# Kernel optimization log

Hardware: AMD Instinct MI355X
Metric: run time of the kernel (lower is better)

Reference implementation:

```python
import jax, jax.numpy as jnp
import numpy as np

KH, KW = 3, 3
STRIDE, PAD, DIL = 1, 1, 1
HEADS, GROUPS, CLIP = 12, 12, 2
C, H, W = 288, 64, 64
B = 2


def _bilinear(img, ys, xs):
    # img: (c, H, W); ys, xs: (K, H, W) fractional sample coords -> (c, K, H, W)
    # DCN-style bilinear with zero outside the image (per-corner validity).
    Hh, Ww = img.shape[1], img.shape[2]
    y0 = jnp.floor(ys)
    x0 = jnp.floor(xs)
    dy = ys - y0
    dx = xs - x0
    out = jnp.zeros((img.shape[0],) + ys.shape, dtype=img.dtype)
    for oy, wy in ((y0, 1.0 - dy), (y0 + 1.0, dy)):
        for ox, wx in ((x0, 1.0 - dx), (x0 + 1.0, dx)):
            valid = (oy >= 0) & (oy <= Hh - 1) & (ox >= 0) & (ox <= Ww - 1)
            yi = jnp.clip(oy, 0, Hh - 1).astype(jnp.int32)
            xi = jnp.clip(ox, 0, Ww - 1).astype(jnp.int32)
            out = out + img[:, yi, xi] * (wy * wx * valid.astype(img.dtype))[None]
    return out


_sample = jax.vmap(jax.vmap(jax.vmap(_bilinear)))  # over (B, T, G)


def _linear5d(x, Wm, b):
    # x: (n, d, c, h, w); Wm: (out, in); torch nn.Linear applied channel-last
    return jnp.einsum('ndchw,oc->ndohw', x, Wm) + b[None, None, :, None, None]


def _deform_attn(q, kv, offset):
    # q: (B,1,C,H,W); kv: (B,T,2C,H,W); offset: (B, T*G*K*2, H, W)
    K = KH * KW
    hd = C // HEADS
    cpg = C // GROUPS
    scale = hd ** -0.5
    A = H * W
    off = offset.reshape(B, CLIP, GROUPS, K, 2, H, W)
    ky = jnp.repeat(jnp.arange(KH), KW).astype(q.dtype)   # (K,)
    kx = jnp.tile(jnp.arange(KW), KH).astype(q.dtype)
    py = jnp.arange(H, dtype=q.dtype)
    px = jnp.arange(W, dtype=q.dtype)
    base_y = ky[:, None, None] * DIL - PAD + py[None, :, None] * STRIDE  # (K,H,1)
    base_x = kx[:, None, None] * DIL - PAD + px[None, None, :] * STRIDE  # (K,1,W)
    ys = base_y + off[..., 0, :, :]  # (B,T,G,K,H,W)
    xs = base_x + off[..., 1, :, :]
    # split kv into k/v, group channels so k and v share per-group offsets
    k_in = kv[:, :, :C].reshape(B, CLIP, GROUPS, cpg, H, W)
    v_in = kv[:, :, C:].reshape(B, CLIP, GROUPS, cpg, H, W)
    kv_g = jnp.concatenate([k_in, v_in], axis=3)          # (B,T,G,2*cpg,H,W)
    samp = _sample(kv_g, ys, xs)                          # (B,T,G,2*cpg,K,H,W)
    k_s = samp[:, :, :, :cpg]
    v_s = samp[:, :, :, cpg:]
    # (B,T,G,cpg,K,H,W) -> (B,HEADS,hd,T*K,A)
    def to_heads(t):
        t = t.reshape(B, CLIP, C, K, A).transpose(0, 2, 1, 3, 4)
        return t.reshape(B, HEADS, hd, CLIP * K, A)
    k_s = to_heads(k_s)
    v_s = to_heads(v_s)
    q_r = q.reshape(B, HEADS, hd, A) * jnp.asarray(scale, q.dtype)
    attn = jnp.einsum('bhda,bhdka->bhka', q_r, k_s)       # (B,HEADS,T*K,A)
    attn = jax.nn.softmax(attn, axis=2)
    out = jnp.einsum('bhka,bhdka->bhda', attn, v_s)
    return out.reshape(B, 1, C, H, W)


def setup_inputs() -> dict:
    key = jax.random.key(0)
    ks = jax.random.split(key, 16)
    s = 0.02
    inp = {
        'q': jax.random.normal(ks[0], (B, 1, C, H, W), jnp.float32),
        'k': jax.random.normal(ks[1], (B, CLIP, C, H, W), jnp.float32),
        'v': jax.random.normal(ks[2], (B, CLIP, C, H, W), jnp.float32),
        'offset': jax.random.normal(ks[3], (B, CLIP * GROUPS * KH * KW * 2, H, W), jnp.float32),
        'Wq': jax.random.normal(ks[4], (C, C), jnp.float32) * s,
        'bq': jnp.zeros((C,), jnp.float32),
        'Wk': jax.random.normal(ks[5], (C, C), jnp.float32) * s,
        'bk': jnp.zeros((C,), jnp.float32),
        'Wv': jax.random.normal(ks[6], (C, C), jnp.float32) * s,
        'bv': jnp.zeros((C,), jnp.float32),
        'W1': jax.random.normal(ks[7], (2 * C, C), jnp.float32) * s,
        'b1': jnp.zeros((2 * C,), jnp.float32),
        'W2': jax.random.normal(ks[8], (C, 2 * C), jnp.float32) * s,
        'b2': jnp.zeros((C,), jnp.float32),
    }
    return inp


def reference(q, k, v, offset, Wq, bq, Wk, bk, Wv, bv, W1, b1, W2, b2):
    qp = _linear5d(q, Wq, bq)
    kv = jnp.concatenate([_linear5d(k, Wk, bk), _linear5d(v, Wv, bv)], axis=2)
    o = _deform_attn(qp, kv, offset)
    # MLP (channel-last), residual: v = v + mlp(v)
    x = jnp.moveaxis(o, 2, -1)
    x = jnp.einsum('ndhwc,oc->ndhwo', x, W1) + b1
    x = jax.nn.gelu(x, approximate=False)
    x = jnp.einsum('ndhwc,oc->ndhwo', x, W2) + b2
    return o + jnp.moveaxis(x, -1, 2)
```

## Files before the change

kernel.cpp:

```cpp
#include <hip/hip_runtime.h>

#define AREA 4096

typedef short short8 __attribute__((ext_vector_type(8)));
typedef float f32x4 __attribute__((ext_vector_type(4)));

__device__ __forceinline__ unsigned bf16_rn(float x) {
    unsigned u = __builtin_bit_cast(unsigned, x);
    u += 0x7fffu + ((u >> 16) & 1u);
    return u >> 16;
}
__device__ __forceinline__ float bflo(unsigned u) { return __builtin_bit_cast(float, u << 16); }
__device__ __forceinline__ float bfhi(unsigned u) { return __builtin_bit_cast(float, u & 0xffff0000u); }
__device__ __forceinline__ float gelu_f(float x) {
    return 0.5f * x * (1.f + erff(x * 0.70710678118654752f));
}

#define OFF_Q 0
#define OFF_K (162 * 64)
#define OFF_V (324 * 64)
#define OFF_1 (486 * 64)
#define OFF_2 (810 * 64)

__global__ __launch_bounds__(256) void prep_kernel(
    const float* __restrict__ q, const float* __restrict__ k,
    const float* __restrict__ v,
    const float* __restrict__ Wq, const float* __restrict__ Wk,
    const float* __restrict__ Wv, const float* __restrict__ W1,
    const float* __restrict__ W2,
    unsigned* __restrict__ xq, unsigned* __restrict__ xk,
    unsigned* __restrict__ xv, uint4* __restrict__ wp)
{
    if (blockIdx.y < 3) {
        const float* src; unsigned* dst; int nimg;
        switch (blockIdx.y) {
            case 0: src = q; dst = xq; nimg = 2; break;
            case 1: src = k; dst = xk; nimg = 4; break;
            default:src = v; dst = xv; nimg = 4; break;
        }
        int idx = blockIdx.x * 256 + threadIdx.x;
        if (idx >= nimg * AREA * 36) return;
        int a = idx & (AREA - 1);
        int rest = idx >> 12;
        int oct = rest % 36;
        int n = rest / 36;
        const float* s = src + ((long)n * 288 + oct * 8) * AREA + a;
        uint4 u;
        u.x = bf16_rn(s[0])        | (bf16_rn(s[AREA])     << 16);
        u.y = bf16_rn(s[2 * AREA]) | (bf16_rn(s[3 * AREA]) << 16);
        u.z = bf16_rn(s[4 * AREA]) | (bf16_rn(s[5 * AREA]) << 16);
        u.w = bf16_rn(s[6 * AREA]) | (bf16_rn(s[7 * AREA]) << 16);
        *(uint4*)(dst + ((long)n * AREA + a) * 144 + oct * 4) = u;
    } else {
        int gw = blockIdx.x * 4 + (threadIdx.x >> 6);
        if (gw >= 1134) return;
        int lane = threadIdx.x & 63;
        const float* W; int Cin, KS, local, off;
        if      (gw < 162) { W = Wq; Cin = 288; KS = 9;  local = gw;       off = OFF_Q; }
        else if (gw < 324) { W = Wk; Cin = 288; KS = 9;  local = gw - 162; off = OFF_K; }
        else if (gw < 486) { W = Wv; Cin = 288; KS = 9;  local = gw - 324; off = OFF_V; }
        else if (gw < 810) { W = W1; Cin = 288; KS = 9;  local = gw - 486; off = OFF_1; }
        else               { W = W2; Cin = 576; KS = 18; local = gw - 810; off = OFF_2; }
        int ot = local / KS, ks = local - ot * KS;
        int o = ot * 16 + (lane & 15);
        int c0 = ks * 32 + ((lane >> 4) << 3);
        const float4* wr = (const float4*)(W + (long)o * Cin + c0);
        float4 f0 = wr[0], f1 = wr[1];
        uint4 u;
        u.x = bf16_rn(f0.x) | (bf16_rn(f0.y) << 16);
        u.y = bf16_rn(f0.z) | (bf16_rn(f0.w) << 16);
        u.z = bf16_rn(f1.x) | (bf16_rn(f1.y) << 16);
        u.w = bf16_rn(f1.z) | (bf16_rn(f1.w) << 16);
        wp[(long)off + (long)local * 64 + lane] = u;
    }
}

__global__ __launch_bounds__(256) void proj_qkv(
    const unsigned* __restrict__ xq, const unsigned* __restrict__ xk,
    const unsigned* __restrict__ xv, const uint4* __restrict__ wp,
    const float* __restrict__ bq, const float* __restrict__ bk,
    const float* __restrict__ bv, unsigned* __restrict__ qp_u,
    unsigned* __restrict__ kv_u)
{
    const int z = blockIdx.z;
    const unsigned* Xt; const uint4* Wp; const float* bias;
    int outmode, voff, n;
    if (z < 2)      { Xt = xq; Wp = wp + OFF_Q; bias = bq; outmode = 1; voff = 0;  n = z; }
    else if (z < 6) { Xt = xk; Wp = wp + OFF_K; bias = bk; outmode = 2; voff = 0;  n = z - 2; }
    else            { Xt = xv; Wp = wp + OFF_V; bias = bv; outmode = 2; voff = 12; n = z - 6; }

    const int tid = threadIdx.x;
    const int lane = tid & 63;
    const int w = tid >> 6;
    const int ot0 = blockIdx.y * 2;
    const int pw = blockIdx.x * 256 + w * 64;
    const int lcol = lane & 15;
    const int lrow = lane >> 4;

    const uint4* xrow[4];
#pragma unroll
    for (int s = 0; s < 4; ++s)
        xrow[s] = (const uint4*)(Xt + ((long)n * AREA + pw + s * 16 + lcol) * 144);
    const uint4* wa0 = Wp + (long)ot0 * 9 * 64 + lane;
    const uint4* wa1 = Wp + (long)(ot0 + 1) * 9 * 64 + lane;

    f32x4 acc[2][4];
#pragma unroll
    for (int m = 0; m < 2; ++m)
#pragma unroll
        for (int s = 0; s < 4; ++s) acc[m][s] = (f32x4){0.f, 0.f, 0.f, 0.f};

    for (int ks = 0; ks < 9; ++ks) {
        uint4 a0 = wa0[(long)ks * 64];
        uint4 a1 = wa1[(long)ks * 64];
        uint4 b[4];
#pragma unroll
        for (int s = 0; s < 4; ++s) b[s] = xrow[s][ks * 4 + lrow];
        short8 A0 = __builtin_bit_cast(short8, a0);
        short8 A1 = __builtin_bit_cast(short8, a1);
#pragma unroll
        for (int s = 0; s < 4; ++s) {
            short8 B = __builtin_bit_cast(short8, b[s]);
            acc[0][s] = __builtin_amdgcn_mfma_f32_16x16x32_bf16(A0, B, acc[0][s], 0, 0, 0);
            acc[1][s] = __builtin_amdgcn_mfma_f32_16x16x32_bf16(A1, B, acc[1][s], 0, 0, 0);
        }
    }

#pragma unroll
    for (int m = 0; m < 2; ++m) {
        const int obase = (ot0 + m) * 16 + lrow * 4;
        const float b0 = bias[obase], b1 = bias[obase + 1];
        const float b2 = bias[obase + 2], b3 = bias[obase + 3];
#pragma unroll
        for (int s = 0; s < 4; ++s) {
            const int pcol = pw + s * 16 + lcol;
            f32x4 a = acc[m][s];
            float v0 = a[0] + b0, v1 = a[1] + b1, v2 = a[2] + b2, v3 = a[3] + b3;
            uint2 st;
            st.x = bf16_rn(v0) | (bf16_rn(v1) << 16);
            st.y = bf16_rn(v2) | (bf16_rn(v3) << 16);
            if (outmode == 1) {
                *(uint2*)(qp_u + ((long)n * AREA + pcol) * 144 + (obase >> 1)) = st;
            } else {
                int g = obase / 24, d0 = obase % 24;
                *(uint2*)(kv_u + ((long)(n * 12 + g) * AREA + pcol) * 24 + voff + (d0 >> 1)) = st;
            }
        }
    }
}

template<int OUT>
__global__ __launch_bounds__(64) void proj_mfma(
    const unsigned* __restrict__ Xt, const uint4* __restrict__ Wp,
    const float* __restrict__ bias, void* __restrict__ outp,
    const unsigned* __restrict__ res_u, int KS, int RSu)
{
    const int lane = threadIdx.x;
    const int n = blockIdx.z;
    const int ot0 = blockIdx.y * 2;
    const int pw = blockIdx.x * 64;
    const int lcol = lane & 15;
    const int lrow = lane >> 4;

    const uint4* xrow[4];
#pragma unroll
    for (int s = 0; s < 4; ++s)
        xrow[s] = (const uint4*)(Xt + ((long)n * AREA + pw + s * 16 + lcol) * RSu);
    const uint4* wa0 = Wp + (long)ot0 * KS * 64 + lane;
    const uint4* wa1 = Wp + (long)(ot0 + 1) * KS * 64 + lane;

    f32x4 acc[2][4];
#pragma unroll
    for (int m = 0; m < 2; ++m)
#pragma unroll
        for (int s = 0; s < 4; ++s) acc[m][s] = (f32x4){0.f, 0.f, 0.f, 0.f};

    for (int ks = 0; ks < KS; ++ks) {
        uint4 a0 = wa0[(long)ks * 64];
        uint4 a1 = wa1[(long)ks * 64];
        uint4 b[4];
#pragma unroll
        for (int s = 0; s < 4; ++s) b[s] = xrow[s][ks * 4 + lrow];
        short8 A0 = __builtin_bit_cast(short8, a0);
        short8 A1 = __builtin_bit_cast(short8, a1);
#pragma unroll
        for (int s = 0; s < 4; ++s) {
            short8 B = __builtin_bit_cast(short8, b[s]);
            acc[0][s] = __builtin_amdgcn_mfma_f32_16x16x32_bf16(A0, B, acc[0][s], 0, 0, 0);
            acc[1][s] = __builtin_amdgcn_mfma_f32_16x16x32_bf16(A1, B, acc[1][s], 0, 0, 0);
        }
    }

#pragma unroll
    for (int m = 0; m < 2; ++m) {
        const int obase = (ot0 + m) * 16 + lrow * 4;
        const float b0 = bias[obase], b1 = bias[obase + 1];
        const float b2 = bias[obase + 2], b3 = bias[obase + 3];
#pragma unroll
        for (int s = 0; s < 4; ++s) {
            const int pcol = pw + s * 16 + lcol;
            f32x4 a = acc[m][s];
            float v0 = a[0] + b0, v1 = a[1] + b1, v2 = a[2] + b2, v3 = a[3] + b3;
            if (OUT == 3) {
                v0 = gelu_f(v0); v1 = gelu_f(v1); v2 = gelu_f(v2); v3 = gelu_f(v3);
                uint2 st;
                st.x = bf16_rn(v0) | (bf16_rn(v1) << 16);
                st.y = bf16_rn(v2) | (bf16_rn(v3) << 16);
                *(uint2*)((unsigned*)outp + ((long)n * AREA + pcol) * 288 + (obase >> 1)) = st;
            } else {
                uint2 rr = *(const uint2*)(res_u + ((long)n * AREA + pcol) * 144 + (obase >> 1));
                float* fb = (float*)outp;
                float vals[4] = {v0 + bflo(rr.x), v1 + bfhi(rr.x),
                                 v2 + bflo(rr.y), v3 + bfhi(rr.y)};
#pragma unroll
                for (int r = 0; r < 4; ++r) {
                    long addr = ((long)n * 288 + obase + r) * AREA + pcol;
                    fb[addr] = vals[r];
                }
            }
        }
    }
}

__global__ __launch_bounds__(256) void deform_attn_kernel(
    const unsigned* __restrict__ qp, const unsigned* __restrict__ kv,
    const float* __restrict__ offs, unsigned* __restrict__ ot)
{
    const int bid = blockIdx.x;
    const int swz = (bid & 7) * 192 + (bid >> 3);
    const int t = swz * 256 + threadIdx.x;
    const int role = t & 1;
    const int clip = (t >> 1) & 1;
    const int site = t >> 2;
    const int a = site & (AREA - 1);
    const int g = (site >> 12) % 12;
    const int b = site / (12 * AREA);
    const int py = a >> 6, px = a & 63;
    const float scale = 0.20412414523193150818f;

    float qv[24];
    {
        const uint4* qb = (const uint4*)(qp + ((long)b * AREA + a) * 144 + g * 12);
        uint4 q0 = qb[0], q1 = qb[1], q2 = qb[2];
        unsigned uq[12] = {q0.x, q0.y, q0.z, q0.w, q1.x, q1.y, q1.z, q1.w,
                           q2.x, q2.y, q2.z, q2.w};
#pragma unroll
        for (int j = 0; j < 12; ++j) {
            qv[2 * j]     = bflo(uq[j]) * scale;
            qv[2 * j + 1] = bfhi(uq[j]) * scale;
        }
    }

    float m = -1e30f, l = 0.f;
    float outv[24];
#pragma unroll
    for (int d = 0; d < 24; ++d) outv[d] = 0.f;

    const unsigned* __restrict__ cb =
        kv + (long)((b * 2 + clip) * 12 + g) * AREA * 24 + role * 12;
    const float* __restrict__ obase =
        offs + ((long)b * 432 + (clip * 12 + g) * 18) * AREA;
#pragma unroll 3
    for (int k = 0; k < 9; ++k) {
        float oy = obase[(long)(2 * k) * AREA + a];
        float ox = obase[(long)(2 * k + 1) * AREA + a];
        int ky = k / 3, kx = k - ky * 3;
        float ys = (float)(py + ky - 1) + oy;
        float xs_ = (float)(px + kx - 1) + ox;
        float y0f = floorf(ys), x0f = floorf(xs_);
        float dy = ys - y0f, dx = xs_ - x0f;
        float wy[2] = {1.f - dy, dy};
        float wx[2] = {1.f - dx, dx};
        long  idx4[4];
        float w4[4];
#pragma unroll
        for (int cy = 0; cy < 2; ++cy) {
            float yc = y0f + (float)cy;
            bool vy = (yc >= 0.f) && (yc <= 63.f);
            int yi = (int)fminf(fmaxf(yc, 0.f), 63.f);
#pragma unroll
            for (int cx = 0; cx < 2; ++cx) {
                float xc = x0f + (float)cx;
                bool vx = (xc >= 0.f) && (xc <= 63.f);
                int xi = (int)fminf(fmaxf(xc, 0.f), 63.f);
                w4[cy * 2 + cx] = wy[cy] * wx[cx] * ((vy && vx) ? 1.f : 0.f);
                idx4[cy * 2 + cx] = (long)(yi * 64 + xi) * 24;
            }
        }
        float xs[24];
#pragma unroll
        for (int j = 0; j < 24; ++j) xs[j] = 0.f;
        float sh = 0.f;
#pragma unroll
        for (int c = 0; c < 4; ++c) {
            const uint4* pc = (const uint4*)(cb + idx4[c]);
            uint4 u0 = pc[0], u1 = pc[1], u2 = pc[2];
            unsigned uu[12] = {u0.x, u0.y, u0.z, u0.w,
                               u1.x, u1.y, u1.z, u1.w,
                               u2.x, u2.y, u2.z, u2.w};
            float w = w4[c];
            float d = 0.f;
#pragma unroll
            for (int j = 0; j < 12; ++j) {
                float lo = bflo(uu[j]), hi = bfhi(uu[j]);
                d = fmaf(qv[2 * j], lo, d);
                d = fmaf(qv[2 * j + 1], hi, d);
                xs[2 * j]     = fmaf(w, lo, xs[2 * j]);
                xs[2 * j + 1] = fmaf(w, hi, xs[2 * j + 1]);
            }
            sh = fmaf(w, d, sh);
        }
        float sx = __shfl_xor(sh, 1);
        float s = role ? sx : sh;
        float mn = fmaxf(m, s);
        float corr = __expf(m - mn);
        float p = __expf(s - mn);
        l = l * corr + p;
        m = mn;
#pragma unroll
        for (int j = 0; j < 24; ++j)
            outv[j] = fmaf(outv[j], corr, p * xs[j]);
    }

    float mo  = __shfl_xor(m, 2);
    float lo2 = __shfl_xor(l, 2);
    float mn = fmaxf(m, mo);
    float fs = __expf(m - mn), fo = __expf(mo - mn);
    float lm = l * fs + lo2 * fo;
    float inv = 1.f / lm;
#pragma unroll
    for (int d = 0; d < 24; ++d) {
        float ovo = __shfl_xor(outv[d], 2);
        outv[d] = (outv[d] * fs + ovo * fo) * inv;
    }

    if (role == 1 && clip == 0) {
        unsigned* tb = ot + ((long)b * AREA + a) * 144 + g * 12;
        uint4 s0, s1, s2;
        s0.x = bf16_rn(outv[0])  | (bf16_rn(outv[1])  << 16);
        s0.y = bf16_rn(outv[2])  | (bf16_rn(outv[3])  << 16);
        s0.z = bf16_rn(outv[4])  | (bf16_rn(outv[5])  << 16);
        s0.w = bf16_rn(outv[6])  | (bf16_rn(outv[7])  << 16);
        s1.x = bf16_rn(outv[8])  | (bf16_rn(outv[9])  << 16);
        s1.y = bf16_rn(outv[10]) | (bf16_rn(outv[11]) << 16);
        s1.z = bf16_rn(outv[12]) | (bf16_rn(outv[13]) << 16);
        s1.w = bf16_rn(outv[14]) | (bf16_rn(outv[15]) << 16);
        s2.x = bf16_rn(outv[16]) | (bf16_rn(outv[17]) << 16);
        s2.y = bf16_rn(outv[18]) | (bf16_rn(outv[19]) << 16);
        s2.z = bf16_rn(outv[20]) | (bf16_rn(outv[21]) << 16);
        s2.w = bf16_rn(outv[22]) | (bf16_rn(outv[23]) << 16);
        ((uint4*)tb)[0] = s0; ((uint4*)tb)[1] = s1; ((uint4*)tb)[2] = s2;
    }
}

extern "C" void kernel_launch(void* const* d_in, const int* in_sizes, int n_in,
                              void* d_out, int out_size, void* d_ws, size_t ws_size,
                              hipStream_t stream) {
    const float* q      = (const float*)d_in[0];
    const float* k      = (const float*)d_in[1];
    const float* v      = (const float*)d_in[2];
    const float* offset = (const float*)d_in[3];
    const float* Wq     = (const float*)d_in[4];
    const float* bq     = (const float*)d_in[5];
    const float* Wk     = (const float*)d_in[6];
    const float* bk     = (const float*)d_in[7];
    const float* Wv     = (const float*)d_in[8];
    const float* bv     = (const float*)d_in[9];
    const float* W1     = (const float*)d_in[10];
    const float* b1     = (const float*)d_in[11];
    const float* W2     = (const float*)d_in[12];
    const float* b2     = (const float*)d_in[13];
    float* out = (float*)d_out;
    float* ws  = (float*)d_ws;

    unsigned* qp_u = (unsigned*)ws;
    unsigned* kv_u = (unsigned*)(ws + 2359296);
    unsigned* xq   = (unsigned*)(ws + 7077888);
    unsigned* xk   = (unsigned*)(ws + 8257536);
    unsigned* xv   = (unsigned*)(ws + 10616832);
    uint4*    wp   = (uint4*)(ws + 12976128);
    unsigned* x1   = xk;
    unsigned* o_t  = xv;

    prep_kernel<<<dim3(2304, 4), dim3(256), 0, stream>>>(
        q, k, v, Wq, Wk, Wv, W1, W2, xq, xk, xv, wp);
    proj_qkv<<<dim3(16, 9, 10), dim3(256), 0, stream>>>(
        xq, xk, xv, wp, bq, bk, bv, qp_u, kv_u);
    deform_attn_kernel<<<dim3(1536), dim3(256), 0, stream>>>(
        qp_u, kv_u, offset, o_t);
    proj_mfma<3><<<dim3(64, 18, 2), dim3(64), 0, stream>>>(
        o_t, wp + OFF_1, b1, x1, nullptr, 9, 144);
    proj_mfma<0><<<dim3(64, 9, 2), dim3(64), 0, stream>>>(
        x1, wp + OFF_2, b2, out, o_t, 18, 288);
}
```

Before: 124.1 us.

## Transpose activations through LDS into K-slab layout for QKV projection

```diff
diff --git a/kernel.cpp b/kernel.cpp
--- a/kernel.cpp
+++ b/kernel.cpp
@@ -31,26 +31,36 @@
     unsigned* __restrict__ xq, unsigned* __restrict__ xk,
     unsigned* __restrict__ xv, uint4* __restrict__ wp)
 {
-    if (blockIdx.y < 3) {
-        const float* src; unsigned* dst; int nimg;
-        switch (blockIdx.y) {
-            case 0: src = q; dst = xq; nimg = 2; break;
-            case 1: src = k; dst = xk; nimg = 4; break;
-            default:src = v; dst = xv; nimg = 4; break;
-        }
-        int idx = blockIdx.x * 256 + threadIdx.x;
-        if (idx >= nimg * AREA * 36) return;
-        int a = idx & (AREA - 1);
-        int rest = idx >> 12;
-        int oct = rest % 36;
-        int n = rest / 36;
-        const float* s = src + ((long)n * 288 + oct * 8) * AREA + a;
-        uint4 u;
-        u.x = bf16_rn(s[0])        | (bf16_rn(s[AREA])     << 16);
-        u.y = bf16_rn(s[2 * AREA]) | (bf16_rn(s[3 * AREA]) << 16);
-        u.z = bf16_rn(s[4 * AREA]) | (bf16_rn(s[5 * AREA]) << 16);
-        u.w = bf16_rn(s[6 * AREA]) | (bf16_rn(s[7 * AREA]) << 16);
-        *(uint4*)(dst + ((long)n * AREA + a) * 144 + oct * 4) = u;
+    if (blockIdx.y == 0) {
+        __shared__ unsigned lds[32 * 145];
+        const int x = blockIdx.x;
+        const int img = x >> 7;
+        const int px0 = (x & 127) * 32;
+        const float* src; unsigned* dst; int n;
+        if (img < 2)      { src = q; dst = xq; n = img; }
+        else if (img < 6) { src = k; dst = xk; n = img - 2; }
+        else              { src = v; dst = xv; n = img - 6; }
+        const int t = threadIdx.x;
+        const int px = t & 31;
+        const int ci0 = t >> 5;
+        const float* sb = src + (long)n * 288 * AREA + px0 + px;
+#pragma unroll
+        for (int j = 0; j < 18; ++j) {
+            int ci = ci0 + j * 8;
+            float a = sb[(long)(2 * ci) * AREA];
+            float b = sb[(long)(2 * ci + 1) * AREA];
+            lds[px * 145 + ci] = bf16_rn(a) | (bf16_rn(b) << 16);
+        }
+        __syncthreads();
+        const int px2 = t >> 3;
+        const int off = (t & 7) * 2;
+#pragma unroll
+        for (int ks = 0; ks < 9; ++ks) {
+            uint2 v2;
+            v2.x = lds[px2 * 145 + ks * 16 + off];
+            v2.y = lds[px2 * 145 + ks * 16 + off + 1];
+            *(uint2*)(dst + (((long)n * 9 + ks) * AREA + px0 + px2) * 16 + off) = v2;
+        }
     } else {
         int gw = blockIdx.x * 4 + (threadIdx.x >> 6);
         if (gw >= 1134) return;
@@ -97,10 +107,7 @@
     const int lcol = lane & 15;
     const int lrow = lane >> 4;
 
-    const uint4* xrow[4];
-#pragma unroll
-    for (int s = 0; s < 4; ++s)
-        xrow[s] = (const uint4*)(Xt + ((long)n * AREA + pw + s * 16 + lcol) * 144);
+    const uint4* Xb = (const uint4*)Xt + (long)n * 9 * AREA * 4;
     const uint4* wa0 = Wp + (long)ot0 * 9 * 64 + lane;
     const uint4* wa1 = Wp + (long)(ot0 + 1) * 9 * 64 + lane;
 
@@ -113,9 +120,11 @@
     for (int ks = 0; ks < 9; ++ks) {
         uint4 a0 = wa0[(long)ks * 64];
         uint4 a1 = wa1[(long)ks * 64];
+        const uint4* xk4 = Xb + (long)ks * AREA * 4;
         uint4 b[4];
 #pragma unroll
-        for (int s = 0; s < 4; ++s) b[s] = xrow[s][ks * 4 + lrow];
+        for (int s = 0; s < 4; ++s)
+            b[s] = xk4[(long)(pw + s * 16 + lcol) * 4 + lrow];
         short8 A0 = __builtin_bit_cast(short8, a0);
         short8 A1 = __builtin_bit_cast(short8, a1);
 #pragma unroll
@@ -382,7 +391,7 @@
     unsigned* x1   = xk;
     unsigned* o_t  = xv;
 
-    prep_kernel<<<dim3(2304, 4), dim3(256), 0, stream>>>(
+    prep_kernel<<<dim3(1280, 2), dim3(256), 0, stream>>>(
         q, k, v, Wq, Wk, Wv, W1, W2, xq, xk, xv, wp);
     proj_qkv<<<dim3(16, 9, 10), dim3(256), 0, stream>>>(
         xq, xk, xv, wp, bq, bk, bv, qp_u, kv_u);
```

Result: faster. 114.8 us (-7.5%).
